# Kernel tuning notes

Measured on AMD Instinct MI355X. Metric: run time of the kernel, lower is better.

The kernel has to match this reference:

```python
import jax, jax.numpy as jnp
import numpy as np

N = 100000   # nodes
E = 1600000  # edges (before self-loops)
C = 128      # num_node_features == graph_hidden_channels (residuals require equality)
NHID = 512
NOUT = 256
B = 512      # number of graphs in the batch
BN_EPS = 1e-5


def setup_inputs() -> dict:
    key = jax.random.key(0)
    ks = list(jax.random.split(key, 32))
    k = iter(ks)

    def w(shape, fan_in):
        return jax.random.normal(next(k), shape, jnp.float32) * (1.0 / np.sqrt(fan_in))

    inp = {}
    inp["x"] = jax.random.normal(next(k), (N, C), jnp.float32)
    inp["edge_index"] = jax.random.randint(next(k), (2, E), 0, N, jnp.int32)
    inp["batch"] = jnp.sort(jax.random.randint(next(k), (N,), 0, B, jnp.int32))
    # three GCN layers: lin weight [C,C], bias [C], BN gamma/beta
    for i in (1, 2, 3):
        inp[f"W{i}"] = w((C, C), C)
        inp[f"b{i}"] = jnp.zeros((C,), jnp.float32)
        inp[f"g{i}"] = jnp.ones((C,), jnp.float32)
        inp[f"be{i}"] = jnp.zeros((C,), jnp.float32)
    # GAT (1 head)
    inp["Wa"] = w((C, C), C)
    inp["asrc"] = w((C,), C)
    inp["adst"] = w((C,), C)
    inp["ba"] = jnp.zeros((C,), jnp.float32)
    inp["ga"] = jnp.ones((C,), jnp.float32)
    inp["bea"] = jnp.zeros((C,), jnp.float32)
    # MLP head
    inp["Wh1"] = w((C, NHID), C)
    inp["bh1"] = jnp.zeros((NHID,), jnp.float32)
    inp["Wm0"] = w((NHID, NHID), NHID)
    inp["bm0"] = jnp.zeros((NHID,), jnp.float32)
    inp["Wm1"] = w((NHID, NHID), NHID)
    inp["bm1"] = jnp.zeros((NHID,), jnp.float32)
    inp["Wo"] = w((NHID, NOUT), NHID)
    inp["bo"] = jnp.zeros((NOUT,), jnp.float32)
    return inp


def _add_self_loops(edge_index):
    loops = jnp.arange(N, dtype=edge_index.dtype)
    src = jnp.concatenate([edge_index[0], loops])
    dst = jnp.concatenate([edge_index[1], loops])
    return src, dst


def _gcn(x, src, dst, W, b):
    # PyG GCNConv: add self-loops, D^-1/2 (A+I) D^-1/2 (x W) + b
    deg = jax.ops.segment_sum(jnp.ones_like(dst, jnp.float32), dst, num_segments=N)
    dinv = jax.lax.rsqrt(jnp.maximum(deg, 1.0))
    norm = dinv[src] * dinv[dst]                      # [E+N]
    h = x @ W                                         # [N,C]
    msg = h[src] * norm[:, None]                      # gather + scale
    return jax.ops.segment_sum(msg, dst, num_segments=N) + b


def _gat(x, src, dst, W, asrc, adst, b):
    # PyG GATConv, heads=1: self-loops, alpha = softmax_dst(leaky_relu(a_s.h_j + a_d.h_i))
    h = x @ W                                         # [N,C]
    es = (h * asrc).sum(-1)                           # [N]
    ed = (h * adst).sum(-1)
    e = jax.nn.leaky_relu(es[src] + ed[dst], 0.2)     # [E+N]
    m = jax.ops.segment_max(e, dst, num_segments=N)
    ex = jnp.exp(e - m[dst])
    s = jax.ops.segment_sum(ex, dst, num_segments=N)
    alpha = ex / (s[dst] + 1e-16)
    out = jax.ops.segment_sum(h[src] * alpha[:, None], dst, num_segments=N)
    return out + b


def _bn(h, g, be):
    # BatchNorm in training mode: biased batch stats over node dim
    m = h.mean(0)
    v = ((h - m) ** 2).mean(0)
    return (h - m) * jax.lax.rsqrt(v + BN_EPS) * g + be


def reference(x, edge_index, batch,
              W1, b1, g1, be1, W2, b2, g2, be2, W3, b3, g3, be3,
              Wa, asrc, adst, ba, ga, bea,
              Wh1, bh1, Wm0, bm0, Wm1, bm1, Wo, bo):
    src, dst = _add_self_loops(edge_index)
    x = jax.nn.relu(_bn(_gcn(x, src, dst, W1, b1), g1, be1)) + x
    x = jax.nn.relu(_bn(_gcn(x, src, dst, W2, b2), g2, be2)) + x
    x = jax.nn.relu(_bn(_gcn(x, src, dst, W3, b3), g3, be3)) + x
    x = jax.nn.relu(_bn(_gat(x, src, dst, Wa, asrc, adst, ba), ga, bea)) + x
    # global mean pool over graphs
    sums = jax.ops.segment_sum(x, batch, num_segments=B)
    cnt = jax.ops.segment_sum(jnp.ones((N,), jnp.float32), batch, num_segments=B)
    x = sums / jnp.maximum(cnt, 1.0)[:, None]         # [B,C]
    x = jax.nn.relu(x @ Wh1 + bh1)
    x = jax.nn.relu(x @ Wm0 + bm0)
    x = jax.nn.relu(x @ Wm1 + bm1)
    return x @ Wo + bo                                # [B,NOUT]
```

## Files before the change

kernel.cpp:

```cpp
#include <hip/hip_runtime.h>
#include <hip/hip_fp16.h>

#define N_NODES 100000
#define N_EDGES 1600000
#define CCH     128
#define BG      512
#define NHID    512
#define NOUT    256
#define BN_EPS  1e-5f
#define CSR_CAP (N_EDGES + 4 * N_NODES + 128)

typedef __attribute__((ext_vector_type(8))) short s16x8;
typedef __attribute__((ext_vector_type(4))) float f32x4;

static __device__ __forceinline__ float leaky(float x) { return x > 0.f ? x : 0.2f * x; }
static __device__ __forceinline__ uint32_t bfr16(float x) {
  uint32_t u = __float_as_uint(x);
  u += 0x7fffu + ((u >> 16) & 1u);
  return u >> 16;
}
static __device__ __forceinline__ uint32_t pack2(float a, float b) {
  return bfr16(a) | (bfr16(b) << 16);
}
static __device__ __forceinline__ float blo(uint32_t u) { return __uint_as_float(u << 16); }
static __device__ __forceinline__ float bhi(uint32_t u) { return __uint_as_float(u & 0xffff0000u); }
static __device__ __forceinline__ uint32_t packh2(float a, float b) {
  __half2 h;
  h.x = __float2half(a);
  h.y = __float2half(b);
  return *reinterpret_cast<uint32_t*>(&h);
}
static __device__ __forceinline__ float hlo(uint32_t u) {
  __half2 h = *reinterpret_cast<__half2*>(&u);
  return __half2float(h.x);
}
static __device__ __forceinline__ float hhi(uint32_t u) {
  __half2 h = *reinterpret_cast<__half2*>(&u);
  return __half2float(h.y);
}

__global__ void hist_kernel(const int* __restrict__ dst, int* __restrict__ indeg) {
  int e = blockIdx.x * 256 + threadIdx.x;
  if (e < N_EDGES) atomicAdd(&indeg[dst[e]], 1);
}

__global__ __launch_bounds__(256) void scan_chunks(const int* __restrict__ indeg,
                                                   int* __restrict__ rowstart,
                                                   int* __restrict__ chunksum) {
  int tid = threadIdx.x;
  int base = blockIdx.x * 1024 + tid * 4;
  int4 v;
  if (base + 3 < N_NODES) {
    v = *(const int4*)(indeg + base);
  } else {
    v.x = (base + 0 < N_NODES) ? indeg[base + 0] : 0;
    v.y = (base + 1 < N_NODES) ? indeg[base + 1] : 0;
    v.z = (base + 2 < N_NODES) ? indeg[base + 2] : 0;
    v.w = (base + 3 < N_NODES) ? indeg[base + 3] : 0;
  }
  int px = (v.x + 3) & ~3, py = (v.y + 3) & ~3, pz = (v.z + 3) & ~3, pw = (v.w + 3) & ~3;
  int s = px + py + pz + pw;
  __shared__ int ss[256];
  ss[tid] = s;
  __syncthreads();
  for (int off = 1; off < 256; off <<= 1) {
    int t = (tid >= off) ? ss[tid - off] : 0;
    __syncthreads();
    ss[tid] += t;
    __syncthreads();
  }
  int excl = ss[tid] - s;
  if (base + 0 < N_NODES) rowstart[base + 0] = excl;
  if (base + 1 < N_NODES) rowstart[base + 1] = excl + px;
  if (base + 2 < N_NODES) rowstart[base + 2] = excl + px + py;
  if (base + 3 < N_NODES) rowstart[base + 3] = excl + px + py + pz;
  if (tid == 255) chunksum[blockIdx.x] = ss[255];
}

__global__ void scan_sums(int* __restrict__ chunksum, int nch, int* __restrict__ totalp) {
  __shared__ int ss[128];
  int tid = threadIdx.x;
  int v = (tid < nch) ? chunksum[tid] : 0;
  ss[tid] = v;
  __syncthreads();
  for (int off = 1; off < 128; off <<= 1) {
    int t = (tid >= off) ? ss[tid - off] : 0;
    __syncthreads();
    ss[tid] += t;
    __syncthreads();
  }
  if (tid < nch) chunksum[tid] = ss[tid] - v;
  if (tid == nch - 1) *totalp = ss[tid];
}

__global__ void scan_add_dinv(int* __restrict__ rowstart, const int* __restrict__ chunksum,
                              const int* __restrict__ indeg, float* __restrict__ dinv) {
  int i = blockIdx.x * 256 + threadIdx.x;
  if (i < N_NODES) {
    rowstart[i] += chunksum[i >> 10];
    dinv[i] = rsqrtf((float)(indeg[i] + 1));
  }
}

__global__ void scatter_edges(const int* __restrict__ src, const int* __restrict__ dst,
                              const int* __restrict__ rowstart, int* __restrict__ cursor,
                              const float* __restrict__ dinv, int2* __restrict__ csr_sw) {
  int e = blockIdx.x * 256 + threadIdx.x;
  if (e < N_EDGES) {
    int d = dst[e];
    int s = src[e];
    int p = rowstart[d] + atomicAdd(&cursor[d], 1);
    float w = dinv[s] * dinv[d];
    csr_sw[p] = make_int2(s, __float_as_int(w));
  }
}

__global__ void prep_kernel(const float2* __restrict__ x2, uint32_t* __restrict__ xb,
                            const float* __restrict__ W1, const float* __restrict__ W2,
                            const float* __restrict__ W3, const float* __restrict__ W4,
                            unsigned short* __restrict__ Wp1, unsigned short* __restrict__ Wp2,
                            unsigned short* __restrict__ Wp3, unsigned short* __restrict__ Wp4) {
  int b = blockIdx.x;
  if (b < 25000) {
    size_t idx = (size_t)b * 256 + threadIdx.x;
    float2 v = x2[idx];
    xb[idx] = pack2(v.x, v.y);
    return;
  }
  int pb = b - 25000;
  int wsel = pb >> 3;
  int t = (pb & 7) * 256 + threadIdx.x;
  const float* W = (wsel == 0) ? W1 : (wsel == 1) ? W2 : (wsel == 2) ? W3 : W4;
  unsigned short* Wp = (wsel == 0) ? Wp1 : (wsel == 1) ? Wp2 : (wsel == 2) ? Wp3 : Wp4;
  int lane = t & 63;
  int ks = (t >> 6) & 3;
  int nt = t >> 8;
  int c = nt * 16 + (lane & 15);
  int kb = ks * 32 + (lane >> 4) * 8;
#pragma unroll
  for (int i = 0; i < 8; ++i)
    Wp[(size_t)t * 8 + i] = (unsigned short)bfr16(W[(size_t)(kb + i) * 128 + c]);
}

__global__ void pack_mlp(const float* __restrict__ Wh1, const float* __restrict__ Wm0,
                         const float* __restrict__ Wm1, const float* __restrict__ Wo,
                         unsigned short* __restrict__ P1, unsigned short* __restrict__ P2,
                         unsigned short* __restrict__ P3, unsigned short* __restrict__ P4) {
  int t = blockIdx.x * 256 + threadIdx.x;
  const float* W;
  unsigned short* P;
  int K, N, loc;
  if (t < 8192)        { W = Wh1; P = P1; K = 128; N = 512; loc = t; }
  else if (t < 40960)  { W = Wm0; P = P2; K = 512; N = 512; loc = t - 8192; }
  else if (t < 73728)  { W = Wm1; P = P3; K = 512; N = 512; loc = t - 40960; }
  else if (t < 90112)  { W = Wo;  P = P4; K = 512; N = 256; loc = t - 73728; }
  else return;
  int ksn = K >> 5;
  int lane = loc & 63;
  int ks = (loc >> 6) & (ksn - 1);
  int nt = loc / (64 * ksn);
  int c = nt * 16 + (lane & 15);
  int kb = ks * 32 + (lane >> 4) * 8;
#pragma unroll
  for (int i = 0; i < 8; ++i)
    P[(size_t)loc * 8 + i] = (unsigned short)bfr16(W[(size_t)(kb + i) * N + c]);
}

template <int FUSE>
__global__ __launch_bounds__(256) void gemm_mfma(uint32_t* __restrict__ xbm,
                                                 const uint32_t* __restrict__ aggb,
                                                 const float* __restrict__ stats,
                                                 const float* __restrict__ gamma,
                                                 const float* __restrict__ beta,
                                                 const unsigned short* __restrict__ Wp,
                                                 uint32_t* __restrict__ Hb,
                                                 int M) {
  __shared__ float scs[128], bcs[128];
  if (FUSE) {
    int t = threadIdx.x;
    if (t < 128) {
      const float n_inv = 1.f / (float)N_NODES;
      float m = stats[t] * n_inv;
      float v = stats[128 + t] * n_inv - m * m;
      float s = gamma[t] * rsqrtf(v + BN_EPS);
      scs[t] = s;
      bcs[t] = beta[t] - m * s;
    }
    __syncthreads();
  }
  int wave = threadIdx.x >> 6, lane = threadIdx.x & 63;
  int row0 = blockIdx.x * 128 + wave * 32;
  int r = lane & 15, g = lane >> 4;

  f32x4 acc[2][8];
#pragma unroll
  for (int mt = 0; mt < 2; ++mt)
#pragma unroll
    for (int nt = 0; nt < 8; ++nt) acc[mt][nt] = (f32x4){0.f, 0.f, 0.f, 0.f};

  s16x8 a[2][4];
#pragma unroll
// ... 69 lines not shown
                                                int M, int K, int N) {
  int wave = threadIdx.x >> 6, lane = threadIdx.x & 63;
  int row0 = blockIdx.x * 128 + wave * 32;
  int colb = blockIdx.y;
  const unsigned short* A16 = (const unsigned short*)Ab;
  int KS = K >> 5;
  int r = lane & 15, g = lane >> 4;
  f32x4 acc[2][8];
#pragma unroll
  for (int mt = 0; mt < 2; ++mt)
#pragma unroll
    for (int nt = 0; nt < 8; ++nt) acc[mt][nt] = (f32x4){0.f, 0.f, 0.f, 0.f};

  for (int ks = 0; ks < KS; ++ks) {
    s16x8 a[2];
#pragma unroll
    for (int mt = 0; mt < 2; ++mt) {
      int row = row0 + mt * 16 + r;
      s16x8 af = {0, 0, 0, 0, 0, 0, 0, 0};
      if (row < M) af = *(const s16x8*)(A16 + (size_t)row * K + ks * 32 + g * 8);
      a[mt] = af;
    }
#pragma unroll
    for (int ntl = 0; ntl < 8; ++ntl) {
      int ntg = colb * 8 + ntl;
      s16x8 b = *(const s16x8*)(Wp + ((size_t)(ntg * KS + ks) * 64 + lane) * 8);
      acc[0][ntl] = __builtin_amdgcn_mfma_f32_16x16x32_bf16(a[0], b, acc[0][ntl], 0, 0, 0);
      acc[1][ntl] = __builtin_amdgcn_mfma_f32_16x16x32_bf16(a[1], b, acc[1][ntl], 0, 0, 0);
    }
  }
#pragma unroll
  for (int mt = 0; mt < 2; ++mt) {
#pragma unroll
    for (int ntl = 0; ntl < 8; ++ntl) {
#pragma unroll
      for (int reg = 0; reg < 4; ++reg) {
        int row = row0 + mt * 16 + (lane >> 4) * 4 + reg;
        int col = colb * 128 + ntl * 16 + (lane & 15);
        float v0 = acc[mt][ntl][reg] + bias[col];
        if (RELU) v0 = fmaxf(v0, 0.f);
        if (OUTF32) {
          if (row < M) ((float*)outp)[(size_t)row * N + col] = v0;
        } else {
          float v1 = __shfl_xor(v0, 1);
          if (!(lane & 1) && row < M)
            ((uint32_t*)outp)[(size_t)row * (N >> 1) + (col >> 1)] = pack2(v0, v1);
        }
      }
    }
  }
}

template <int GAT>
__global__ __launch_bounds__(256) void agg_kernel(const uint2* __restrict__ Hb2,
                                                  const int* __restrict__ rowstart,
                                                  const int2* __restrict__ pack,
                                                  const float* __restrict__ dinv,
                                                  const int* __restrict__ indeg,
                                                  const float* __restrict__ es,
                                                  const float* __restrict__ ed,
                                                  uint32_t* __restrict__ aggb,
                                                  float* __restrict__ stats) {
  const float INVALW = GAT ? -1e30f : 0.0f;
  int tid = threadIdx.x;
  int lane = tid & 63;
  int hl = lane & 31;
  int half = lane >> 5;
  int gw = (blockIdx.x * 256 + tid) >> 6;
  int nw = (gridDim.x * 256) >> 6;
  float s0 = 0, s1 = 0, s2 = 0, s3 = 0, q0 = 0, q1 = 0, q2 = 0, q3 = 0;

#define LOADPK(gq, I0, I1, I2, I3, V0, V1, V2, V3)                        \
  do {                                                                    \
    bool ok = (gq) < G;                                                   \
    int ee = e0 + (gq) * 4;                                               \
    int2 pa = pack[ee], pb = pack[ee + 1], pc = pack[ee + 2], pd = pack[ee + 3]; \
    I0 = ok ? pa.x : 0; V0 = ok ? __int_as_float(pa.y) : INVALW;          \
    I1 = ok ? pb.x : 0; V1 = ok ? __int_as_float(pb.y) : INVALW;          \
    I2 = ok ? pc.x : 0; V2 = ok ? __int_as_float(pc.y) : INVALW;          \
    I3 = ok ? pd.x : 0; V3 = ok ? __int_as_float(pd.y) : INVALW;          \
  } while (0)

  for (int pi = gw; pi < N_NODES / 2; pi += nw) {
    int n = 2 * pi + half;
    int e0 = rowstart[n], e1p = rowstart[n + 1];
    int G = (e1p - e0) >> 2;
    int Gmax = max(G, __shfl_xor(G, 32));
    float edi = 0.f, selfw, fscale = 1.f;
    if (GAT) {
      int len = indeg[n];
      edi = ed[n];
      float wself = __expf(leaky(es[n] + edi));
      float wsum = (hl == 0) ? wself : 0.f;
      for (int e = e0 + hl; e < e0 + len; e += 32)
        wsum += __expf(leaky(__int_as_float(pack[e].y) + edi));
#pragma unroll
      for (int off = 16; off; off >>= 1) wsum += __shfl_xor(wsum, off);
      fscale = 1.f / (wsum + 1e-16f);
      selfw = wself;
    } else {
      float di = dinv[n];
      selfw = di * di;
    }
    uint2 hs = Hb2[(size_t)n * 32 + hl];
    float c0 = blo(hs.x) * selfw, c1 = bhi(hs.x) * selfw;
    float c2 = blo(hs.y) * selfw, c3 = bhi(hs.y) * selfw;

    if (Gmax > 0) {
      int j0, j1, j2, j3;
      float wC0, wC1, wC2, wC3;
      float wB0, wB1, wB2, wB3;
      float wA0, wA1, wA2, wA3;
      uint2 R00, R01, R02, R03;
      uint2 R10, R11, R12, R13;
      LOADPK(0, j0, j1, j2, j3, wC0, wC1, wC2, wC3);
      R00 = Hb2[(size_t)(unsigned)j0 * 32 + hl];
      R01 = Hb2[(size_t)(unsigned)j1 * 32 + hl];
      R02 = Hb2[(size_t)(unsigned)j2 * 32 + hl];
      R03 = Hb2[(size_t)(unsigned)j3 * 32 + hl];
      LOADPK(1, j0, j1, j2, j3, wB0, wB1, wB2, wB3);
      R10 = Hb2[(size_t)(unsigned)j0 * 32 + hl];
      R11 = Hb2[(size_t)(unsigned)j1 * 32 + hl];
      R12 = Hb2[(size_t)(unsigned)j2 * 32 + hl];
      R13 = Hb2[(size_t)(unsigned)j3 * 32 + hl];
      LOADPK(2, j0, j1, j2, j3, wA0, wA1, wA2, wA3);
      for (int g = 0; g < Gmax; ++g) {
        uint2 R20, R21, R22, R23;
        if (g + 2 < Gmax) {
          R20 = Hb2[(size_t)(unsigned)j0 * 32 + hl];
          R21 = Hb2[(size_t)(unsigned)j1 * 32 + hl];
          R22 = Hb2[(size_t)(unsigned)j2 * 32 + hl];
          R23 = Hb2[(size_t)(unsigned)j3 * 32 + hl];
        }
        int k0, k1, k2, k3;
        float wN0, wN1, wN2, wN3;
        if (g + 3 < Gmax) {
          LOADPK(g + 3, k0, k1, k2, k3, wN0, wN1, wN2, wN3);
        } else {
          k0 = k1 = k2 = k3 = 0;
          wN0 = wN1 = wN2 = wN3 = INVALW;
        }
        float f0, f1, f2, f3;
        if (GAT) {
          f0 = __expf(leaky(wC0 + edi)); f1 = __expf(leaky(wC1 + edi));
          f2 = __expf(leaky(wC2 + edi)); f3 = __expf(leaky(wC3 + edi));
        } else {
          f0 = wC0; f1 = wC1; f2 = wC2; f3 = wC3;
        }
        __builtin_amdgcn_s_setprio(1);
        c0 = fmaf(blo(R00.x), f0, c0); c1 = fmaf(bhi(R00.x), f0, c1);
        c2 = fmaf(blo(R00.y), f0, c2); c3 = fmaf(bhi(R00.y), f0, c3);
        c0 = fmaf(blo(R01.x), f1, c0); c1 = fmaf(bhi(R01.x), f1, c1);
        c2 = fmaf(blo(R01.y), f1, c2); c3 = fmaf(bhi(R01.y), f1, c3);
        c0 = fmaf(blo(R02.x), f2, c0); c1 = fmaf(bhi(R02.x), f2, c1);
        c2 = fmaf(blo(R02.y), f2, c2); c3 = fmaf(bhi(R02.y), f2, c3);
        c0 = fmaf(blo(R03.x), f3, c0); c1 = fmaf(bhi(R03.x), f3, c1);
        c2 = fmaf(blo(R03.y), f3, c2); c3 = fmaf(bhi(R03.y), f3, c3);
        __builtin_amdgcn_s_setprio(0);
        R00 = R10; R01 = R11; R02 = R12; R03 = R13;
        R10 = R20; R11 = R21; R12 = R22; R13 = R23;
        wC0 = wB0; wC1 = wB1; wC2 = wB2; wC3 = wB3;
        wB0 = wA0; wB1 = wA1; wB2 = wA2; wB3 = wA3;
        wA0 = wN0; wA1 = wN1; wA2 = wN2; wA3 = wN3;
        j0 = k0; j1 = k1; j2 = k2; j3 = k3;
      }
    }
    if (GAT) { c0 *= fscale; c1 *= fscale; c2 *= fscale; c3 *= fscale; }
    ((uint2*)aggb)[(size_t)n * 32 + hl] = make_uint2(packh2(c0, c1), packh2(c2, c3));
    s0 += c0; s1 += c1; s2 += c2; s3 += c3;
    q0 += c0 * c0; q1 += c1 * c1; q2 += c2 * c2; q3 += c3 * c3;
  }
#undef LOADPK
  s0 += __shfl_xor(s0, 32); s1 += __shfl_xor(s1, 32);
  s2 += __shfl_xor(s2, 32); s3 += __shfl_xor(s3, 32);
  q0 += __shfl_xor(q0, 32); q1 += __shfl_xor(q1, 32);
  q2 += __shfl_xor(q2, 32); q3 += __shfl_xor(q3, 32);
  __shared__ float red[4][128];
  int w = tid >> 6;
  if (half == 0) {
    red[w][4 * hl + 0] = s0; red[w][4 * hl + 1] = s1;
    red[w][4 * hl + 2] = s2; red[w][4 * hl + 3] = s3;
  }
  __syncthreads();
  if (w == 0) {
    float a = red[0][2 * lane] + red[1][2 * lane] + red[2][2 * lane] + red[3][2 * lane];
    float b = red[0][2 * lane + 1] + red[1][2 * lane + 1] + red[2][2 * lane + 1] + red[3][2 * lane + 1];
    atomicAdd(&stats[2 * lane], a);
    atomicAdd(&stats[2 * lane + 1], b);
  }
  __syncthreads();
  if (half == 0) {
    red[w][4 * hl + 0] = q0; red[w][4 * hl + 1] = q1;
    red[w][4 * hl + 2] = q2; red[w][4 * hl + 3] = q3;
  }
  __syncthreads();
  if (w == 0) {
    float a = red[0][2 * lane] + red[1][2 * lane] + red[2][2 * lane] + red[3][2 * lane];
    float b = red[0][2 * lane + 1] + red[1][2 * lane + 1] + red[2][2 * lane + 1] + red[3][2 * lane + 1];
    atomicAdd(&stats[128 + 2 * lane], a);
    atomicAdd(&stats[128 + 2 * lane + 1], b);
  }
}

__global__ __launch_bounds__(256) void compute_esed(const uint32_t* __restrict__ Hb,
                                                    const float* __restrict__ asrc,
                                                    const float* __restrict__ adst,
                                                    float* __restrict__ es, float* __restrict__ ed) {
  int lane = threadIdx.x & 63;
  int gwave = (blockIdx.x * 256 + threadIdx.x) >> 6;
  if (gwave >= N_NODES) return;
  float2 av = ((const float2*)asrc)[lane];
  float2 dv = ((const float2*)adst)[lane];
  uint32_t hv = Hb[(size_t)gwave * 64 + lane];
  float hx = blo(hv), hy = bhi(hv);
  float e_s = hx * av.x + hy * av.y;
  float e_d = hx * dv.x + hy * dv.y;
  for (int off = 32; off; off >>= 1) {
    e_s += __shfl_down(e_s, off);
    e_d += __shfl_down(e_d, off);
  }
  if (lane == 0) { es[gwave] = e_s; ed[gwave] = e_d; }
}

__global__ void gat_pack_kernel(int2* __restrict__ sw, const float* __restrict__ es) {
  int e = blockIdx.x * 256 + threadIdx.x;
// ... 41 lines not shown
  }
  __shared__ float red[256];
  __shared__ float fin[128];
  red[threadIdx.x] = acc;
  __syncthreads();
  if (half == 0) {
    float vsum = red[c] + red[128 + c];
    int cnt = e - s;
    fin[c] = vsum / fmaxf((float)cnt, 1.f);
  }
  __syncthreads();
  if (half == 0 && !(c & 1))
    pooledb[(size_t)g * 64 + (c >> 1)] = pack2(fin[c], fin[c + 1]);
}

extern "C" void kernel_launch(void* const* d_in, const int* in_sizes, int n_in,
                              void* d_out, int out_size, void* d_ws, size_t ws_size,
                              hipStream_t stream) {
  const float* x_in  = (const float*)d_in[0];
  const int*   eidx  = (const int*)d_in[1];
  const int*   batch = (const int*)d_in[2];
  const float* W1 = (const float*)d_in[3];
  const float* g1 = (const float*)d_in[5];
  const float* be1 = (const float*)d_in[6];
  const float* W2 = (const float*)d_in[7];
  const float* g2 = (const float*)d_in[9];
  const float* be2 = (const float*)d_in[10];
  const float* W3 = (const float*)d_in[11];
  const float* g3 = (const float*)d_in[13];
  const float* be3 = (const float*)d_in[14];
  const float* Wa = (const float*)d_in[15];
  const float* asrc = (const float*)d_in[16];
  const float* adst = (const float*)d_in[17];
  const float* ga = (const float*)d_in[19];
  const float* bea = (const float*)d_in[20];
  const float* Wh1 = (const float*)d_in[21];
  const float* bh1 = (const float*)d_in[22];
  const float* Wm0 = (const float*)d_in[23];
  const float* bm0 = (const float*)d_in[24];
  const float* Wm1 = (const float*)d_in[25];
  const float* bm1 = (const float*)d_in[26];
  const float* Wo = (const float*)d_in[27];
  const float* bo = (const float*)d_in[28];

  const int* src = eidx;
  const int* dst = eidx + N_EDGES;

  char* p = (char*)d_ws;
  auto alloc = [&](size_t bytes) {
    char* r = p;
    p += (bytes + 255) & ~(size_t)255;
    return r;
  };
  uint32_t* Hb     = (uint32_t*)alloc((size_t)N_NODES * 64 * 4);
  uint32_t* xb     = (uint32_t*)alloc((size_t)N_NODES * 64 * 4);
  uint32_t* aggb   = (uint32_t*)alloc((size_t)N_NODES * 64 * 4);
  int2*  csr_sw    = (int2*)alloc((size_t)CSR_CAP * 8);
  int*   rowstart  = (int*)alloc((size_t)(N_NODES + 1) * 4);
  int*   indeg     = (int*)alloc((size_t)2 * N_NODES * 4);
  int*   cursor    = indeg + N_NODES;
  float* dinv      = (float*)alloc((size_t)N_NODES * 4);
  float* es        = (float*)alloc((size_t)N_NODES * 4);
  float* ed        = (float*)alloc((size_t)N_NODES * 4);
  int*   chunksum  = (int*)alloc(128 * 4);
  float* stats     = (float*)alloc(4 * 256 * 4);
  int*   gstart    = (int*)alloc((BG + 1) * 4);
  uint32_t* pooledb = (uint32_t*)alloc((size_t)BG * 64 * 4);
  uint32_t* m1b    = (uint32_t*)alloc((size_t)BG * (NHID / 2) * 4);
  uint32_t* m2b    = (uint32_t*)alloc((size_t)BG * (NHID / 2) * 4);
  unsigned short* Wp1 = (unsigned short*)alloc(2048 * 8 * 2);
  unsigned short* Wp2 = (unsigned short*)alloc(2048 * 8 * 2);
  unsigned short* Wp3 = (unsigned short*)alloc(2048 * 8 * 2);
  unsigned short* Wp4 = (unsigned short*)alloc(2048 * 8 * 2);
  unsigned short* P1 = (unsigned short*)alloc((size_t)8192 * 8 * 2);
  unsigned short* P2 = (unsigned short*)alloc((size_t)32768 * 8 * 2);
  unsigned short* P3 = (unsigned short*)alloc((size_t)32768 * 8 * 2);
  unsigned short* P4 = (unsigned short*)alloc((size_t)16384 * 8 * 2);

  hipMemsetAsync(indeg, 0, (size_t)2 * N_NODES * 4, stream);
  hipMemsetAsync(stats, 0, 4 * 256 * 4, stream);
  hipMemsetAsync(csr_sw, 0, (size_t)CSR_CAP * 8, stream);

  hist_kernel<<<(N_EDGES + 255) / 256, 256, 0, stream>>>(dst, indeg);
  scan_chunks<<<98, 256, 0, stream>>>(indeg, rowstart, chunksum);
  scan_sums<<<1, 128, 0, stream>>>(chunksum, 98, rowstart + N_NODES);
  scan_add_dinv<<<(N_NODES + 255) / 256, 256, 0, stream>>>(rowstart, chunksum, indeg, dinv);
  scatter_edges<<<(N_EDGES + 255) / 256, 256, 0, stream>>>(src, dst, rowstart, cursor, dinv, csr_sw);

  prep_kernel<<<25000 + 32, 256, 0, stream>>>((const float2*)x_in, xb, W1, W2, W3, Wa,
                                              Wp1, Wp2, Wp3, Wp4);
  pack_mlp<<<352, 256, 0, stream>>>(Wh1, Wm0, Wm1, Wo, P1, P2, P3, P4);

  const int gemm_blocks_m = (N_NODES + 127) / 128;
  const int AGG_BLOCKS = 2048;

  gemm_mfma<0><<<gemm_blocks_m, 256, 0, stream>>>(xb, nullptr, nullptr, nullptr, nullptr,
                                                  Wp1, Hb, N_NODES);
  agg_kernel<0><<<AGG_BLOCKS, 256, 0, stream>>>((const uint2*)Hb, rowstart, csr_sw, dinv,
                                                indeg, nullptr, nullptr, aggb, stats + 0 * 256);
  gemm_mfma<1><<<gemm_blocks_m, 256, 0, stream>>>(xb, aggb, stats + 0 * 256, g1, be1,
                                                  Wp2, Hb, N_NODES);
  agg_kernel<0><<<AGG_BLOCKS, 256, 0, stream>>>((const uint2*)Hb, rowstart, csr_sw, dinv,
                                                indeg, nullptr, nullptr, aggb, stats + 1 * 256);
  gemm_mfma<1><<<gemm_blocks_m, 256, 0, stream>>>(xb, aggb, stats + 1 * 256, g2, be2,
                                                  Wp3, Hb, N_NODES);
  agg_kernel<0><<<AGG_BLOCKS, 256, 0, stream>>>((const uint2*)Hb, rowstart, csr_sw, dinv,
                                                indeg, nullptr, nullptr, aggb, stats + 2 * 256);
  gemm_mfma<1><<<gemm_blocks_m, 256, 0, stream>>>(xb, aggb, stats + 2 * 256, g3, be3,
                                                  Wp4, Hb, N_NODES);
  compute_esed<<<(N_NODES + 3) / 4, 256, 0, stream>>>(Hb, asrc, adst, es, ed);
  gat_pack_kernel<<<(CSR_CAP + 255) / 256, 256, 0, stream>>>(csr_sw, es);
  agg_kernel<1><<<AGG_BLOCKS, 256, 0, stream>>>((const uint2*)Hb, rowstart, csr_sw, nullptr,
                                                indeg, es, ed, aggb, stats + 3 * 256);

  graph_starts<<<(N_NODES + 255) / 256, 256, 0, stream>>>(batch, gstart);
  pool_bn<<<BG, 256, 0, stream>>>(aggb, xb, stats + 3 * 256, ga, bea, gstart, pooledb);

  gemm_mlp<1, 0><<<dim3(4, 4), 256, 0, stream>>>(pooledb, P1, bh1, m1b, BG, CCH, NHID);
  gemm_mlp<1, 0><<<dim3(4, 4), 256, 0, stream>>>(m1b, P2, bm0, m2b, BG, NHID, NHID);
  gemm_mlp<1, 0><<<dim3(4, 4), 256, 0, stream>>>(m2b, P3, bm1, m1b, BG, NHID, NHID);
  gemm_mlp<0, 1><<<dim3(4, 2), 256, 0, stream>>>(m1b, P4, bo, d_out, BG, NHID, NOUT);
}
```

Before: 1.028 ms.

## Tile neighbor aggregation by source-node range for L2 locality

The CSR build now bins each destination's edges by source tile (8 tiles of 12500 nodes), using per-(node, tile) counts and tile start offsets. The aggregation kernel keeps up to 13 node accumulators per wave in registers and sweeps the source tiles one at a time, so concurrent gathers touch a feature slice small enough to stay in cache. It also switches edge loads and output stores to nontemporal access. In exchange it drops the previous software-pipelined gather loop, leaves very short inner loops per tile, raises register pressure, and adds larger count arrays, memsets and extra preprocessing kernels.

```diff
diff --git a/kernel.cpp b/kernel.cpp
--- a/kernel.cpp
+++ b/kernel.cpp
@@ -9,6 +9,11 @@
 #define NOUT    256
 #define BN_EPS  1e-5f
 #define CSR_CAP (N_EDGES + 4 * N_NODES + 128)
+#define TILE_N  12500
+#define NTILES  8
+#define AGG_BLOCKS 1024
+#define NWAVES  (AGG_BLOCKS * 4)
+#define KMAX    13
 
 typedef __attribute__((ext_vector_type(8))) short s16x8;
 typedef __attribute__((ext_vector_type(4))) float f32x4;
@@ -39,9 +44,24 @@
   return __half2float(h.y);
 }
 
-__global__ void hist_kernel(const int* __restrict__ dst, int* __restrict__ indeg) {
+__global__ void hist2_kernel(const int* __restrict__ src, const int* __restrict__ dst,
+                             int* __restrict__ cnt2) {
   int e = blockIdx.x * 256 + threadIdx.x;
-  if (e < N_EDGES) atomicAdd(&indeg[dst[e]], 1);
+  if (e < N_EDGES) {
+    int t = src[e] / TILE_N;
+    atomicAdd(&cnt2[(size_t)dst[e] * NTILES + t], 1);
+  }
+}
+
+__global__ void deg_dinv_kernel(const int* __restrict__ cnt2, int* __restrict__ indeg,
+                                float* __restrict__ dinv) {
+  int n = blockIdx.x * 256 + threadIdx.x;
+  if (n >= N_NODES) return;
+  int s = 0;
+#pragma unroll
+  for (int t = 0; t < NTILES; ++t) s += cnt2[(size_t)n * NTILES + t];
+  indeg[n] = s;
+  dinv[n] = rsqrtf((float)(s + 1));
 }
 
 __global__ __launch_bounds__(256) void scan_chunks(const int* __restrict__ indeg,
@@ -93,23 +113,33 @@
   if (tid == nch - 1) *totalp = ss[tid];
 }
 
-__global__ void scan_add_dinv(int* __restrict__ rowstart, const int* __restrict__ chunksum,
-                              const int* __restrict__ indeg, float* __restrict__ dinv) {
+__global__ void scan_add(int* __restrict__ rowstart, const int* __restrict__ chunksum) {
   int i = blockIdx.x * 256 + threadIdx.x;
-  if (i < N_NODES) {
-    rowstart[i] += chunksum[i >> 10];
-    dinv[i] = rsqrtf((float)(indeg[i] + 1));
-  }
-}
-
-__global__ void scatter_edges(const int* __restrict__ src, const int* __restrict__ dst,
-                              const int* __restrict__ rowstart, int* __restrict__ cursor,
-                              const float* __restrict__ dinv, int2* __restrict__ csr_sw) {
+  if (i < N_NODES) rowstart[i] += chunksum[i >> 10];
+}
+
+__global__ void tilestart_kernel(const int* __restrict__ rowstart, const int* __restrict__ cnt2,
+                                 int* __restrict__ ts) {
+  int n = blockIdx.x * 256 + threadIdx.x;
+  if (n >= N_NODES) return;
+  int r = rowstart[n];
+#pragma unroll
+  for (int t = 0; t < NTILES; ++t) {
+    ts[(size_t)n * 9 + t] = r;
+    r += cnt2[(size_t)n * NTILES + t];
+  }
+  ts[(size_t)n * 9 + 8] = r;
+}
+
+__global__ void scatter2_kernel(const int* __restrict__ src, const int* __restrict__ dst,
+                                const int* __restrict__ ts, int* __restrict__ cur2,
+                                const float* __restrict__ dinv, int2* __restrict__ csr_sw) {
   int e = blockIdx.x * 256 + threadIdx.x;
   if (e < N_EDGES) {
     int d = dst[e];
     int s = src[e];
-    int p = rowstart[d] + atomicAdd(&cursor[d], 1);
+    int t = s / TILE_N;
+    int p = ts[(size_t)d * 9 + t] + atomicAdd(&cur2[(size_t)d * NTILES + t], 1);
     float w = dinv[s] * dinv[d];
     csr_sw[p] = make_int2(s, __float_as_int(w));
   }
@@ -322,125 +352,126 @@
 }
 
 template <int GAT>
-__global__ __launch_bounds__(256) void agg_kernel(const uint2* __restrict__ Hb2,
-                                                  const int* __restrict__ rowstart,
-                                                  const int2* __restrict__ pack,
-                                                  const float* __restrict__ dinv,
-                                                  const int* __restrict__ indeg,
-                                                  const float* __restrict__ es,
-                                                  const float* __restrict__ ed,
-                                                  uint32_t* __restrict__ aggb,
-                                                  float* __restrict__ stats) {
+__global__ __launch_bounds__(256, 4) void agg_tiled(const uint2* __restrict__ Hb2,
+                                                    const int* __restrict__ rowstart,
+                                                    const int* __restrict__ ts,
+                                                    const int2* __restrict__ pack,
+                                                    const float* __restrict__ dinv,
+                                                    const int* __restrict__ indeg,
+                                                    const float* __restrict__ es,
+                                                    const float* __restrict__ ed,
+                                                    uint32_t* __restrict__ aggb,
+                                                    float* __restrict__ stats) {
   const float INVALW = GAT ? -1e30f : 0.0f;
   int tid = threadIdx.x;
   int lane = tid & 63;
   int hl = lane & 31;
   int half = lane >> 5;
   int gw = (blockIdx.x * 256 + tid) >> 6;
-  int nw = (gridDim.x * 256) >> 6;
+
+  float acc[KMAX][4];
+  float fsc[KMAX];
+
+#pragma unroll
+  for (int k = 0; k < KMAX; ++k) {
+    acc[k][0] = acc[k][1] = acc[k][2] = acc[k][3] = 0.f;
+    fsc[k] = 1.f;
+    int pi = gw + k * NWAVES;
+    if (pi < N_NODES / 2) {
+      int n = 2 * pi + half;
+      float selfw;
+      if (GAT) {
+        float edi = ed[n];
+        float wself = __expf(leaky(es[n] + edi));
+        int e0 = rowstart[n], len = indeg[n];
+        float wsum = (hl == 0) ? wself : 0.f;
+        for (int e = e0 + hl; e < e0 + len; e += 32) {
+          unsigned long long pw =
+              __builtin_nontemporal_load((const unsigned long long*)&pack[e]);
+          wsum += __expf(leaky(__uint_as_float((unsigned)(pw >> 32)) + edi));
+        }
+#pragma unroll
+        for (int off = 16; off; off >>= 1) wsum += __shfl_xor(wsum, off);
+        fsc[k] = 1.f / (wsum + 1e-16f);
+        selfw = wself;
+      } else {
+        float di = dinv[n];
+        selfw = di * di;
+      }
+      uint2 hs = Hb2[(size_t)n * 32 + hl];
+      acc[k][0] = blo(hs.x) * selfw;
+      acc[k][1] = bhi(hs.x) * selfw;
+      acc[k][2] = blo(hs.y) * selfw;
+      acc[k][3] = bhi(hs.y) * selfw;
+    }
+  }
+
+  for (int t = 0; t < NTILES; ++t) {
+#pragma unroll
+    for (int k = 0; k < KMAX; ++k) {
+      int pi = gw + k * NWAVES;
+      if (pi < N_NODES / 2) {
+        int n = 2 * pi + half;
+        int e0 = rowstart[n];
+        int t0 = ts[(size_t)n * 9 + t];
+        int t1 = ts[(size_t)n * 9 + t + 1];
+        int g_lo = (t0 - e0 + 3) >> 2;
+        int g_hi = (t1 - e0 + 3) >> 2;
+        int ln = g_hi - g_lo;
+        int lmax = max(ln, __shfl_xor(ln, 32));
+        float edi = GAT ? ed[n] : 0.f;
+        for (int j = 0; j < lmax; ++j) {
+          bool ok = j < ln;
+          int ee = ok ? (e0 + (g_lo + j) * 4) : e0;
+          unsigned long long p0 = __builtin_nontemporal_load((const unsigned long long*)&pack[ee]);
+          unsigned long long p1 = __builtin_nontemporal_load((const unsigned long long*)&pack[ee + 1]);
+          unsigned long long p2 = __builtin_nontemporal_load((const unsigned long long*)&pack[ee + 2]);
+          unsigned long long p3 = __builtin_nontemporal_load((const unsigned long long*)&pack[ee + 3]);
+          int i0 = (int)(unsigned)p0, i1 = (int)(unsigned)p1;
+          int i2 = (int)(unsigned)p2, i3 = (int)(unsigned)p3;
+          float w0 = ok ? __uint_as_float((unsigned)(p0 >> 32)) : INVALW;
+          float w1 = ok ? __uint_as_float((unsigned)(p1 >> 32)) : INVALW;
+          float w2 = ok ? __uint_as_float((unsigned)(p2 >> 32)) : INVALW;
+          float w3 = ok ? __uint_as_float((unsigned)(p3 >> 32)) : INVALW;
+          uint2 r0 = Hb2[(size_t)(unsigned)i0 * 32 + hl];
+          uint2 r1 = Hb2[(size_t)(unsigned)i1 * 32 + hl];
+          uint2 r2 = Hb2[(size_t)(unsigned)i2 * 32 + hl];
+          uint2 r3 = Hb2[(size_t)(unsigned)i3 * 32 + hl];
+          float f0, f1, f2, f3;
+          if (GAT) {
+            f0 = __expf(leaky(w0 + edi)); f1 = __expf(leaky(w1 + edi));
+            f2 = __expf(leaky(w2 + edi)); f3 = __expf(leaky(w3 + edi));
+          } else {
+            f0 = w0; f1 = w1; f2 = w2; f3 = w3;
+          }
+          acc[k][0] = fmaf(blo(r0.x), f0, acc[k][0]); acc[k][1] = fmaf(bhi(r0.x), f0, acc[k][1]);
+          acc[k][2] = fmaf(blo(r0.y), f0, acc[k][2]); acc[k][3] = fmaf(bhi(r0.y), f0, acc[k][3]);
+          acc[k][0] = fmaf(blo(r1.x), f1, acc[k][0]); acc[k][1] = fmaf(bhi(r1.x), f1, acc[k][1]);
+          acc[k][2] = fmaf(blo(r1.y), f1, acc[k][2]); acc[k][3] = fmaf(bhi(r1.y), f1, acc[k][3]);
+          acc[k][0] = fmaf(blo(r2.x), f2, acc[k][0]); acc[k][1] = fmaf(bhi(r2.x), f2, acc[k][1]);
+          acc[k][2] = fmaf(blo(r2.y), f2, acc[k][2]); acc[k][3] = fmaf(bhi(r2.y), f2, acc[k][3]);
+          acc[k][0] = fmaf(blo(r3.x), f3, acc[k][0]); acc[k][1] = fmaf(bhi(r3.x), f3, acc[k][1]);
+          acc[k][2] = fmaf(blo(r3.y), f3, acc[k][2]); acc[k][3] = fmaf(bhi(r3.y), f3, acc[k][3]);
+        }
+      }
+    }
+  }
+
   float s0 = 0, s1 = 0, s2 = 0, s3 = 0, q0 = 0, q1 = 0, q2 = 0, q3 = 0;
-
-#define LOADPK(gq, I0, I1, I2, I3, V0, V1, V2, V3)                        \
-  do {                                                                    \
-    bool ok = (gq) < G;                                                   \
-    int ee = e0 + (gq) * 4;                                               \
-    int2 pa = pack[ee], pb = pack[ee + 1], pc = pack[ee + 2], pd = pack[ee + 3]; \
-    I0 = ok ? pa.x : 0; V0 = ok ? __int_as_float(pa.y) : INVALW;          \
-    I1 = ok ? pb.x : 0; V1 = ok ? __int_as_float(pb.y) : INVALW;          \
-    I2 = ok ? pc.x : 0; V2 = ok ? __int_as_float(pc.y) : INVALW;          \
-    I3 = ok ? pd.x : 0; V3 = ok ? __int_as_float(pd.y) : INVALW;          \
-  } while (0)
-
-  for (int pi = gw; pi < N_NODES / 2; pi += nw) {
-    int n = 2 * pi + half;
-    int e0 = rowstart[n], e1p = rowstart[n + 1];
-    int G = (e1p - e0) >> 2;
-    int Gmax = max(G, __shfl_xor(G, 32));
-    float edi = 0.f, selfw, fscale = 1.f;
-    if (GAT) {
-      int len = indeg[n];
-      edi = ed[n];
-      float wself = __expf(leaky(es[n] + edi));
-      float wsum = (hl == 0) ? wself : 0.f;
-      for (int e = e0 + hl; e < e0 + len; e += 32)
-        wsum += __expf(leaky(__int_as_float(pack[e].y) + edi));
-#pragma unroll
-      for (int off = 16; off; off >>= 1) wsum += __shfl_xor(wsum, off);
-      fscale = 1.f / (wsum + 1e-16f);
-      selfw = wself;
-    } else {
-      float di = dinv[n];
-      selfw = di * di;
-    }
-    uint2 hs = Hb2[(size_t)n * 32 + hl];
-    float c0 = blo(hs.x) * selfw, c1 = bhi(hs.x) * selfw;
-    float c2 = blo(hs.y) * selfw, c3 = bhi(hs.y) * selfw;
-
-    if (Gmax > 0) {
-      int j0, j1, j2, j3;
-      float wC0, wC1, wC2, wC3;
-      float wB0, wB1, wB2, wB3;
-      float wA0, wA1, wA2, wA3;
-      uint2 R00, R01, R02, R03;
-      uint2 R10, R11, R12, R13;
-      LOADPK(0, j0, j1, j2, j3, wC0, wC1, wC2, wC3);
-      R00 = Hb2[(size_t)(unsigned)j0 * 32 + hl];
-      R01 = Hb2[(size_t)(unsigned)j1 * 32 + hl];
-      R02 = Hb2[(size_t)(unsigned)j2 * 32 + hl];
-      R03 = Hb2[(size_t)(unsigned)j3 * 32 + hl];
-      LOADPK(1, j0, j1, j2, j3, wB0, wB1, wB2, wB3);
-      R10 = Hb2[(size_t)(unsigned)j0 * 32 + hl];
-      R11 = Hb2[(size_t)(unsigned)j1 * 32 + hl];
-      R12 = Hb2[(size_t)(unsigned)j2 * 32 + hl];
-      R13 = Hb2[(size_t)(unsigned)j3 * 32 + hl];
-      LOADPK(2, j0, j1, j2, j3, wA0, wA1, wA2, wA3);
-      for (int g = 0; g < Gmax; ++g) {
-        uint2 R20, R21, R22, R23;
-        if (g + 2 < Gmax) {
-          R20 = Hb2[(size_t)(unsigned)j0 * 32 + hl];
-          R21 = Hb2[(size_t)(unsigned)j1 * 32 + hl];
-          R22 = Hb2[(size_t)(unsigned)j2 * 32 + hl];
-          R23 = Hb2[(size_t)(unsigned)j3 * 32 + hl];
-        }
-        int k0, k1, k2, k3;
-        float wN0, wN1, wN2, wN3;
-        if (g + 3 < Gmax) {
-          LOADPK(g + 3, k0, k1, k2, k3, wN0, wN1, wN2, wN3);
-        } else {
-          k0 = k1 = k2 = k3 = 0;
-          wN0 = wN1 = wN2 = wN3 = INVALW;
-        }
-        float f0, f1, f2, f3;
-        if (GAT) {
-          f0 = __expf(leaky(wC0 + edi)); f1 = __expf(leaky(wC1 + edi));
-          f2 = __expf(leaky(wC2 + edi)); f3 = __expf(leaky(wC3 + edi));
-        } else {
-          f0 = wC0; f1 = wC1; f2 = wC2; f3 = wC3;
-        }
-        __builtin_amdgcn_s_setprio(1);
-        c0 = fmaf(blo(R00.x), f0, c0); c1 = fmaf(bhi(R00.x), f0, c1);
-        c2 = fmaf(blo(R00.y), f0, c2); c3 = fmaf(bhi(R00.y), f0, c3);
-        c0 = fmaf(blo(R01.x), f1, c0); c1 = fmaf(bhi(R01.x), f1, c1);
-        c2 = fmaf(blo(R01.y), f1, c2); c3 = fmaf(bhi(R01.y), f1, c3);
-        c0 = fmaf(blo(R02.x), f2, c0); c1 = fmaf(bhi(R02.x), f2, c1);
-        c2 = fmaf(blo(R02.y), f2, c2); c3 = fmaf(bhi(R02.y), f2, c3);
-        c0 = fmaf(blo(R03.x), f3, c0); c1 = fmaf(bhi(R03.x), f3, c1);
-        c2 = fmaf(blo(R03.y), f3, c2); c3 = fmaf(bhi(R03.y), f3, c3);
-        __builtin_amdgcn_s_setprio(0);
-        R00 = R10; R01 = R11; R02 = R12; R03 = R13;
-        R10 = R20; R11 = R21; R12 = R22; R13 = R23;
-        wC0 = wB0; wC1 = wB1; wC2 = wB2; wC3 = wB3;
-        wB0 = wA0; wB1 = wA1; wB2 = wA2; wB3 = wA3;
-        wA0 = wN0; wA1 = wN1; wA2 = wN2; wA3 = wN3;
-        j0 = k0; j1 = k1; j2 = k2; j3 = k3;
-      }
-    }
-    if (GAT) { c0 *= fscale; c1 *= fscale; c2 *= fscale; c3 *= fscale; }
-    ((uint2*)aggb)[(size_t)n * 32 + hl] = make_uint2(packh2(c0, c1), packh2(c2, c3));
-    s0 += c0; s1 += c1; s2 += c2; s3 += c3;
-    q0 += c0 * c0; q1 += c1 * c1; q2 += c2 * c2; q3 += c3 * c3;
-  }
-#undef LOADPK
+#pragma unroll
+  for (int k = 0; k < KMAX; ++k) {
+    int pi = gw + k * NWAVES;
+    if (pi < N_NODES / 2) {
+      int n = 2 * pi + half;
+      float c0 = acc[k][0], c1 = acc[k][1], c2 = acc[k][2], c3 = acc[k][3];
+      if (GAT) { c0 *= fsc[k]; c1 *= fsc[k]; c2 *= fsc[k]; c3 *= fsc[k]; }
+      unsigned long long ov = (unsigned long long)packh2(c0, c1) |
+                              ((unsigned long long)packh2(c2, c3) << 32);
+      __builtin_nontemporal_store(ov, (unsigned long long*)&aggb[(size_t)n * 64 + 2 * hl]);
+      s0 += c0; s1 += c1; s2 += c2; s3 += c3;
+      q0 += c0 * c0; q1 += c1 * c1; q2 += c2 * c2; q3 += c3 * c3;
+    }
+  }
   s0 += __shfl_xor(s0, 32); s1 += __shfl_xor(s1, 32);
   s2 += __shfl_xor(s2, 32); s3 += __shfl_xor(s3, 32);
   q0 += __shfl_xor(q0, 32); q1 += __shfl_xor(q1, 32);
@@ -593,8 +624,10 @@
   uint32_t* aggb   = (uint32_t*)alloc((size_t)N_NODES * 64 * 4);
   int2*  csr_sw    = (int2*)alloc((size_t)CSR_CAP * 8);
   int*   rowstart  = (int*)alloc((size_t)(N_NODES + 1) * 4);
-  int*   indeg     = (int*)alloc((size_t)2 * N_NODES * 4);
-  int*   cursor    = indeg + N_NODES;
+  int*   cnt2      = (int*)alloc((size_t)2 * N_NODES * NTILES * 4);
+  int*   cur2      = cnt2 + (size_t)N_NODES * NTILES;
+  int*   tsarr     = (int*)alloc((size_t)N_NODES * 9 * 4);
+  int*   indeg     = (int*)alloc((size_t)N_NODES * 4);
   float* dinv      = (float*)alloc((size_t)N_NODES * 4);
   float* es        = (float*)alloc((size_t)N_NODES * 4);
   float* ed        = (float*)alloc((size_t)N_NODES * 4);
@@ -613,41 +646,42 @@
   unsigned short* P3 = (unsigned short*)alloc((size_t)32768 * 8 * 2);
   unsigned short* P4 = (unsigned short*)alloc((size_t)16384 * 8 * 2);
 
-  hipMemsetAsync(indeg, 0, (size_t)2 * N_NODES * 4, stream);
+  hipMemsetAsync(cnt2, 0, (size_t)2 * N_NODES * NTILES * 4, stream);
   hipMemsetAsync(stats, 0, 4 * 256 * 4, stream);
   hipMemsetAsync(csr_sw, 0, (size_t)CSR_CAP * 8, stream);
 
-  hist_kernel<<<(N_EDGES + 255) / 256, 256, 0, stream>>>(dst, indeg);
+  hist2_kernel<<<(N_EDGES + 255) / 256, 256, 0, stream>>>(src, dst, cnt2);
+  deg_dinv_kernel<<<(N_NODES + 255) / 256, 256, 0, stream>>>(cnt2, indeg, dinv);
   scan_chunks<<<98, 256, 0, stream>>>(indeg, rowstart, chunksum);
   scan_sums<<<1, 128, 0, stream>>>(chunksum, 98, rowstart + N_NODES);
-  scan_add_dinv<<<(N_NODES + 255) / 256, 256, 0, stream>>>(rowstart, chunksum, indeg, dinv);
-  scatter_edges<<<(N_EDGES + 255) / 256, 256, 0, stream>>>(src, dst, rowstart, cursor, dinv, csr_sw);
+  scan_add<<<(N_NODES + 255) / 256, 256, 0, stream>>>(rowstart, chunksum);
+  tilestart_kernel<<<(N_NODES + 255) / 256, 256, 0, stream>>>(rowstart, cnt2, tsarr);
+  scatter2_kernel<<<(N_EDGES + 255) / 256, 256, 0, stream>>>(src, dst, tsarr, cur2, dinv, csr_sw);
 
   prep_kernel<<<25000 + 32, 256, 0, stream>>>((const float2*)x_in, xb, W1, W2, W3, Wa,
                                               Wp1, Wp2, Wp3, Wp4);
   pack_mlp<<<352, 256, 0, stream>>>(Wh1, Wm0, Wm1, Wo, P1, P2, P3, P4);
 
   const int gemm_blocks_m = (N_NODES + 127) / 128;
-  const int AGG_BLOCKS = 2048;
 
   gemm_mfma<0><<<gemm_blocks_m, 256, 0, stream>>>(xb, nullptr, nullptr, nullptr, nullptr,
                                                   Wp1, Hb, N_NODES);
-  agg_kernel<0><<<AGG_BLOCKS, 256, 0, stream>>>((const uint2*)Hb, rowstart, csr_sw, dinv,
-                                                indeg, nullptr, nullptr, aggb, stats + 0 * 256);
+  agg_tiled<0><<<AGG_BLOCKS, 256, 0, stream>>>((const uint2*)Hb, rowstart, tsarr, csr_sw,
+                                               dinv, indeg, nullptr, nullptr, aggb, stats + 0 * 256);
   gemm_mfma<1><<<gemm_blocks_m, 256, 0, stream>>>(xb, aggb, stats + 0 * 256, g1, be1,
                                                   Wp2, Hb, N_NODES);
-  agg_kernel<0><<<AGG_BLOCKS, 256, 0, stream>>>((const uint2*)Hb, rowstart, csr_sw, dinv,
-                                                indeg, nullptr, nullptr, aggb, stats + 1 * 256);
+  agg_tiled<0><<<AGG_BLOCKS, 256, 0, stream>>>((const uint2*)Hb, rowstart, tsarr, csr_sw,
+                                               dinv, indeg, nullptr, nullptr, aggb, stats + 1 * 256);
   gemm_mfma<1><<<gemm_blocks_m, 256, 0, stream>>>(xb, aggb, stats + 1 * 256, g2, be2,
                                                   Wp3, Hb, N_NODES);
-  agg_kernel<0><<<AGG_BLOCKS, 256, 0, stream>>>((const uint2*)Hb, rowstart, csr_sw, dinv,
-                                                indeg, nullptr, nullptr, aggb, stats + 2 * 256);
+  agg_tiled<0><<<AGG_BLOCKS, 256, 0, stream>>>((const uint2*)Hb, rowstart, tsarr, csr_sw,
+                                               dinv, indeg, nullptr, nullptr, aggb, stats + 2 * 256);
   gemm_mfma<1><<<gemm_blocks_m, 256, 0, stream>>>(xb, aggb, stats + 2 * 256, g3, be3,
                                                   Wp4, Hb, N_NODES);
   compute_esed<<<(N_NODES + 3) / 4, 256, 0, stream>>>(Hb, asrc, adst, es, ed);
   gat_pack_kernel<<<(CSR_CAP + 255) / 256, 256, 0, stream>>>(csr_sw, es);
-  agg_kernel<1><<<AGG_BLOCKS, 256, 0, stream>>>((const uint2*)Hb, rowstart, csr_sw, nullptr,
-                                                indeg, es, ed, aggb, stats + 3 * 256);
+  agg_tiled<1><<<AGG_BLOCKS, 256, 0, stream>>>((const uint2*)Hb, rowstart, tsarr, csr_sw,
+                                               nullptr, indeg, es, ed, aggb, stats + 3 * 256);
 
   graph_starts<<<(N_NODES + 255) / 256, 256, 0, stream>>>(batch, gstart);
   pool_bn<<<BG, 256, 0, stream>>>(aggb, xb, stats + 3 * 256, ga, bea, gstart, pooledb);
```

New measurement: 1.303 ms. 26.8% more time.

## Sort nodes by degree bucket for aggregation and merge setup kernels

Applied to the files above, without the earlier changes.

Builds a permutation of nodes grouped by in-degree bucket (descending) and has the aggregation kernels process nodes in that order. Paired half-wavefronts then handle nodes with similar edge counts, which is meant to cut divergence from the Gmax loop bound. It also merges the scan-sum and dinv kernels, folds MLP weight packing into the prep kernel, and replaces three memsets with one. The cost is two extra small kernels with atomics, plus scattered, non-coalesced node access and aggb writes in the aggregation.

```diff
diff --git a/kernel.cpp b/kernel.cpp
--- a/kernel.cpp
+++ b/kernel.cpp
@@ -77,28 +77,58 @@
   if (tid == 255) chunksum[blockIdx.x] = ss[255];
 }
 
-__global__ void scan_sums(int* __restrict__ chunksum, int nch, int* __restrict__ totalp) {
+__global__ __launch_bounds__(256) void scan_finish(const int* __restrict__ chunksum,
+                                                   int* __restrict__ rowstart,
+                                                   const int* __restrict__ indeg,
+                                                   float* __restrict__ dinv,
+                                                   int* __restrict__ gcnt) {
   __shared__ int ss[128];
+  __shared__ int ex[128];
   int tid = threadIdx.x;
-  int v = (tid < nch) ? chunksum[tid] : 0;
-  ss[tid] = v;
+  int v0 = 0;
+  if (tid < 128) { v0 = (tid < 98) ? chunksum[tid] : 0; ss[tid] = v0; }
   __syncthreads();
   for (int off = 1; off < 128; off <<= 1) {
-    int t = (tid >= off) ? ss[tid - off] : 0;
+    int t = 0;
+    if (tid < 128 && tid >= off) t = ss[tid - off];
     __syncthreads();
-    ss[tid] += t;
+    if (tid < 128) ss[tid] += t;
     __syncthreads();
   }
-  if (tid < nch) chunksum[tid] = ss[tid] - v;
-  if (tid == nch - 1) *totalp = ss[tid];
-}
-
-__global__ void scan_add_dinv(int* __restrict__ rowstart, const int* __restrict__ chunksum,
-                              const int* __restrict__ indeg, float* __restrict__ dinv) {
-  int i = blockIdx.x * 256 + threadIdx.x;
+  if (tid < 128) ex[tid] = ss[tid] - v0;
+  __syncthreads();
+  int i = blockIdx.x * 256 + tid;
   if (i < N_NODES) {
-    rowstart[i] += chunksum[i >> 10];
-    dinv[i] = rsqrtf((float)(indeg[i] + 1));
+    rowstart[i] += ex[i >> 10];
+    int d = indeg[i];
+    dinv[i] = rsqrtf((float)(d + 1));
+    int g = (d + 3) >> 2;
+    if (g > 63) g = 63;
+    atomicAdd(&gcnt[g], 1);
+  } else if (i == N_NODES) {
+    rowstart[N_NODES] = ss[97];
+  }
+}
+
+__global__ __launch_bounds__(256) void scatter_perm(const int* __restrict__ indeg,
+                                                    const int* __restrict__ gcnt,
+                                                    int* __restrict__ gcur,
+                                                    int* __restrict__ perm) {
+  __shared__ int start[64];
+  int tid = threadIdx.x;
+  if (tid < 64) {
+    int s = 0;
+    for (int j = tid + 1; j < 64; ++j) s += gcnt[j];
+    start[tid] = s;
+  }
+  __syncthreads();
+  int n = blockIdx.x * 256 + tid;
+  if (n < N_NODES) {
+    int d = indeg[n];
+    int g = (d + 3) >> 2;
+    if (g > 63) g = 63;
+    int pos = start[g] + atomicAdd(&gcur[g], 1);
+    perm[pos] = n;
   }
 }
 
@@ -119,7 +149,11 @@
                             const float* __restrict__ W1, const float* __restrict__ W2,
                             const float* __restrict__ W3, const float* __restrict__ W4,
                             unsigned short* __restrict__ Wp1, unsigned short* __restrict__ Wp2,
-                            unsigned short* __restrict__ Wp3, unsigned short* __restrict__ Wp4) {
+                            unsigned short* __restrict__ Wp3, unsigned short* __restrict__ Wp4,
+                            const float* __restrict__ Wh1, const float* __restrict__ Wm0,
+                            const float* __restrict__ Wm1, const float* __restrict__ Wo,
+                            unsigned short* __restrict__ P1, unsigned short* __restrict__ P2,
+                            unsigned short* __restrict__ P3, unsigned short* __restrict__ P4) {
   int b = blockIdx.x;
   if (b < 25000) {
     size_t idx = (size_t)b * 256 + threadIdx.x;
@@ -127,26 +161,23 @@
     xb[idx] = pack2(v.x, v.y);
     return;
   }
-  int pb = b - 25000;
-  int wsel = pb >> 3;
-  int t = (pb & 7) * 256 + threadIdx.x;
-  const float* W = (wsel == 0) ? W1 : (wsel == 1) ? W2 : (wsel == 2) ? W3 : W4;
-  unsigned short* Wp = (wsel == 0) ? Wp1 : (wsel == 1) ? Wp2 : (wsel == 2) ? Wp3 : Wp4;
-  int lane = t & 63;
-  int ks = (t >> 6) & 3;
-  int nt = t >> 8;
-  int c = nt * 16 + (lane & 15);
-  int kb = ks * 32 + (lane >> 4) * 8;
-#pragma unroll
-  for (int i = 0; i < 8; ++i)
-    Wp[(size_t)t * 8 + i] = (unsigned short)bfr16(W[(size_t)(kb + i) * 128 + c]);
-}
-
-__global__ void pack_mlp(const float* __restrict__ Wh1, const float* __restrict__ Wm0,
-                         const float* __restrict__ Wm1, const float* __restrict__ Wo,
-                         unsigned short* __restrict__ P1, unsigned short* __restrict__ P2,
-                         unsigned short* __restrict__ P3, unsigned short* __restrict__ P4) {
-  int t = blockIdx.x * 256 + threadIdx.x;
+  if (b < 25032) {
+    int pb = b - 25000;
+    int wsel = pb >> 3;
+    int t = (pb & 7) * 256 + threadIdx.x;
+    const float* W = (wsel == 0) ? W1 : (wsel == 1) ? W2 : (wsel == 2) ? W3 : W4;
+    unsigned short* Wp = (wsel == 0) ? Wp1 : (wsel == 1) ? Wp2 : (wsel == 2) ? Wp3 : Wp4;
+    int lane = t & 63;
+    int ks = (t >> 6) & 3;
+    int nt = t >> 8;
+    int c = nt * 16 + (lane & 15);
+    int kb = ks * 32 + (lane >> 4) * 8;
+#pragma unroll
+    for (int i = 0; i < 8; ++i)
+      Wp[(size_t)t * 8 + i] = (unsigned short)bfr16(W[(size_t)(kb + i) * 128 + c]);
+    return;
+  }
+  int t = (b - 25032) * 256 + threadIdx.x;
   const float* W;
   unsigned short* P;
   int K, N, loc;
@@ -325,6 +356,7 @@
 __global__ __launch_bounds__(256) void agg_kernel(const uint2* __restrict__ Hb2,
                                                   const int* __restrict__ rowstart,
                                                   const int2* __restrict__ pack,
+                                                  const int* __restrict__ perm,
                                                   const float* __restrict__ dinv,
                                                   const int* __restrict__ indeg,
                                                   const float* __restrict__ es,
@@ -352,7 +384,7 @@
   } while (0)
 
   for (int pi = gw; pi < N_NODES / 2; pi += nw) {
-    int n = 2 * pi + half;
+    int n = perm[2 * pi + half];
     int e0 = rowstart[n], e1p = rowstart[n + 1];
     int G = (e1p - e0) >> 2;
     int Gmax = max(G, __shfl_xor(G, 32));
@@ -588,18 +620,23 @@
     p += (bytes + 255) & ~(size_t)255;
     return r;
   };
+  char* zbase = p;
+  int*   indeg     = (int*)alloc((size_t)2 * N_NODES * 4);
+  int*   cursor    = indeg + N_NODES;
+  float* stats     = (float*)alloc(4 * 256 * 4);
+  int*   gcnt      = (int*)alloc(128 * 4);
+  int*   gcur      = gcnt + 64;
+  int2*  csr_sw    = (int2*)alloc((size_t)CSR_CAP * 8);
+  size_t zsize = (size_t)(p - zbase);
   uint32_t* Hb     = (uint32_t*)alloc((size_t)N_NODES * 64 * 4);
   uint32_t* xb     = (uint32_t*)alloc((size_t)N_NODES * 64 * 4);
   uint32_t* aggb   = (uint32_t*)alloc((size_t)N_NODES * 64 * 4);
-  int2*  csr_sw    = (int2*)alloc((size_t)CSR_CAP * 8);
   int*   rowstart  = (int*)alloc((size_t)(N_NODES + 1) * 4);
-  int*   indeg     = (int*)alloc((size_t)2 * N_NODES * 4);
-  int*   cursor    = indeg + N_NODES;
+  int*   perm      = (int*)alloc((size_t)N_NODES * 4);
   float* dinv      = (float*)alloc((size_t)N_NODES * 4);
   float* es        = (float*)alloc((size_t)N_NODES * 4);
   float* ed        = (float*)alloc((size_t)N_NODES * 4);
   int*   chunksum  = (int*)alloc(128 * 4);
-  float* stats     = (float*)alloc(4 * 256 * 4);
   int*   gstart    = (int*)alloc((BG + 1) * 4);
   uint32_t* pooledb = (uint32_t*)alloc((size_t)BG * 64 * 4);
   uint32_t* m1b    = (uint32_t*)alloc((size_t)BG * (NHID / 2) * 4);
@@ -613,43 +650,41 @@
   unsigned short* P3 = (unsigned short*)alloc((size_t)32768 * 8 * 2);
   unsigned short* P4 = (unsigned short*)alloc((size_t)16384 * 8 * 2);
 
-  hipMemsetAsync(indeg, 0, (size_t)2 * N_NODES * 4, stream);
-  hipMemsetAsync(stats, 0, 4 * 256 * 4, stream);
-  hipMemsetAsync(csr_sw, 0, (size_t)CSR_CAP * 8, stream);
+  hipMemsetAsync(zbase, 0, zsize, stream);
 
   hist_kernel<<<(N_EDGES + 255) / 256, 256, 0, stream>>>(dst, indeg);
   scan_chunks<<<98, 256, 0, stream>>>(indeg, rowstart, chunksum);
-  scan_sums<<<1, 128, 0, stream>>>(chunksum, 98, rowstart + N_NODES);
-  scan_add_dinv<<<(N_NODES + 255) / 256, 256, 0, stream>>>(rowstart, chunksum, indeg, dinv);
+  scan_finish<<<(N_NODES + 256) / 256, 256, 0, stream>>>(chunksum, rowstart, indeg, dinv, gcnt);
+  scatter_perm<<<(N_NODES + 255) / 256, 256, 0, stream>>>(indeg, gcnt, gcur, perm);
   scatter_edges<<<(N_EDGES + 255) / 256, 256, 0, stream>>>(src, dst, rowstart, cursor, dinv, csr_sw);
 
-  prep_kernel<<<25000 + 32, 256, 0, stream>>>((const float2*)x_in, xb, W1, W2, W3, Wa,
-                                              Wp1, Wp2, Wp3, Wp4);
-  pack_mlp<<<352, 256, 0, stream>>>(Wh1, Wm0, Wm1, Wo, P1, P2, P3, P4);
+  prep_kernel<<<25032 + 352, 256, 0, stream>>>((const float2*)x_in, xb, W1, W2, W3, Wa,
+                                               Wp1, Wp2, Wp3, Wp4,
+                                               Wh1, Wm0, Wm1, Wo, P1, P2, P3, P4);
+  graph_starts<<<(N_NODES + 255) / 256, 256, 0, stream>>>(batch, gstart);
 
   const int gemm_blocks_m = (N_NODES + 127) / 128;
   const int AGG_BLOCKS = 2048;
 
   gemm_mfma<0><<<gemm_blocks_m, 256, 0, stream>>>(xb, nullptr, nullptr, nullptr, nullptr,
                                                   Wp1, Hb, N_NODES);
-  agg_kernel<0><<<AGG_BLOCKS, 256, 0, stream>>>((const uint2*)Hb, rowstart, csr_sw, dinv,
-                                                indeg, nullptr, nullptr, aggb, stats + 0 * 256);
+  agg_kernel<0><<<AGG_BLOCKS, 256, 0, stream>>>((const uint2*)Hb, rowstart, csr_sw, perm,
+                                                dinv, indeg, nullptr, nullptr, aggb, stats + 0 * 256);
   gemm_mfma<1><<<gemm_blocks_m, 256, 0, stream>>>(xb, aggb, stats + 0 * 256, g1, be1,
                                                   Wp2, Hb, N_NODES);
-  agg_kernel<0><<<AGG_BLOCKS, 256, 0, stream>>>((const uint2*)Hb, rowstart, csr_sw, dinv,
-                                                indeg, nullptr, nullptr, aggb, stats + 1 * 256);
+  agg_kernel<0><<<AGG_BLOCKS, 256, 0, stream>>>((const uint2*)Hb, rowstart, csr_sw, perm,
+                                                dinv, indeg, nullptr, nullptr, aggb, stats + 1 * 256);
   gemm_mfma<1><<<gemm_blocks_m, 256, 0, stream>>>(xb, aggb, stats + 1 * 256, g2, be2,
                                                   Wp3, Hb, N_NODES);
-  agg_kernel<0><<<AGG_BLOCKS, 256, 0, stream>>>((const uint2*)Hb, rowstart, csr_sw, dinv,
-                                                indeg, nullptr, nullptr, aggb, stats + 2 * 256);
+  agg_kernel<0><<<AGG_BLOCKS, 256, 0, stream>>>((const uint2*)Hb, rowstart, csr_sw, perm,
+                                                dinv, indeg, nullptr, nullptr, aggb, stats + 2 * 256);
   gemm_mfma<1><<<gemm_blocks_m, 256, 0, stream>>>(xb, aggb, stats + 2 * 256, g3, be3,
                                                   Wp4, Hb, N_NODES);
   compute_esed<<<(N_NODES + 3) / 4, 256, 0, stream>>>(Hb, asrc, adst, es, ed);
   gat_pack_kernel<<<(CSR_CAP + 255) / 256, 256, 0, stream>>>(csr_sw, es);
-  agg_kernel<1><<<AGG_BLOCKS, 256, 0, stream>>>((const uint2*)Hb, rowstart, csr_sw, nullptr,
-                                                indeg, es, ed, aggb, stats + 3 * 256);
-
-  graph_starts<<<(N_NODES + 255) / 256, 256, 0, stream>>>(batch, gstart);
+  agg_kernel<1><<<AGG_BLOCKS, 256, 0, stream>>>((const uint2*)Hb, rowstart, csr_sw, perm,
+                                                nullptr, indeg, es, ed, aggb, stats + 3 * 256);
+
   pool_bn<<<BG, 256, 0, stream>>>(aggb, xb, stats + 3 * 256, ga, bea, gstart, pooledb);
 
   gemm_mlp<1, 0><<<dim3(4, 4), 256, 0, stream>>>(pooledb, P1, bh1, m1b, BG, CCH, NHID);
```

Result: slower. 2.162 ms (+110.4%).
